# Kernel tuning notes

Hardware: AMD Instinct MI355X
Metric: run time of the kernel (lower is better)

Reference implementation:

```python
import jax, jax.numpy as jnp
import numpy as np

# Stand-in base model config (HF-style causal LM)
L, D, H, DFF, V, T = 2, 1024, 16, 4096, 32000, 2
HD = D // H
B, S = 2, 1024


def setup_inputs() -> dict:
    key = jax.random.key(0)
    ks = jax.random.split(key, 20)
    s = 0.02
    ds = 0.002  # task-vector deltas are small finetuning differences
    inp = {
        "input_ids": jax.random.randint(ks[0], (B, S), 0, V, dtype=jnp.int32),
        "labels": jax.random.randint(ks[1], (B, S), 0, V, dtype=jnp.int32),
        "lambdas": jax.random.uniform(ks[2], (T,), jnp.float32) * 0.5,
        # base parameters (frozen, like base_model)
        "emb": jax.random.normal(ks[3], (V, D), jnp.float32) * s,
        "Wqkv": jax.random.normal(ks[4], (L, D, 3 * D), jnp.float32) * s,
        "Wo": jax.random.normal(ks[5], (L, D, D), jnp.float32) * s,
        "W1": jax.random.normal(ks[6], (L, D, DFF), jnp.float32) * s,
        "W2": jax.random.normal(ks[7], (L, DFF, D), jnp.float32) * s,
        "g1": jnp.ones((L, D), jnp.float32),
        "g2": jnp.ones((L, D), jnp.float32),
        "gf": jnp.ones((D,), jnp.float32),
        # stacked task-vector deltas: leading dim T (one slice per CPUStoredTaskVector)
        "d_emb": jax.random.normal(ks[8], (T, V, D), jnp.float32) * ds,
        "d_Wqkv": jax.random.normal(ks[9], (T, L, D, 3 * D), jnp.float32) * ds,
        "d_Wo": jax.random.normal(ks[10], (T, L, D, D), jnp.float32) * ds,
        "d_W1": jax.random.normal(ks[11], (T, L, D, DFF), jnp.float32) * ds,
        "d_W2": jax.random.normal(ks[12], (T, L, DFF, D), jnp.float32) * ds,
        "d_g1": jax.random.normal(ks[13], (T, L, D), jnp.float32) * ds,
        "d_g2": jax.random.normal(ks[14], (T, L, D), jnp.float32) * ds,
        "d_gf": jax.random.normal(ks[15], (T, D), jnp.float32) * ds,
    }
    return inp


def _ln(x, g):
    mu = x.mean(-1, keepdims=True)
    var = ((x - mu) ** 2).mean(-1, keepdims=True)
    return (x - mu) * jax.lax.rsqrt(var + 1e-5) * g


def reference(input_ids, labels, lambdas, emb, Wqkv, Wo, W1, W2, g1, g2, gf,
              d_emb, d_Wqkv, d_Wo, d_W1, d_W2, d_g1, d_g2, d_gf):
    # fused layerwise merge: param + sum_i lambdas[i] * delta_i (single pass over all deltas)
    m = lambda base, d: base + jnp.einsum("t,t...->...", lambdas, d)
    emb_m = m(emb, d_emb)
    x = emb_m[input_ids]  # [B, S, D]
    b, s, _ = x.shape
    causal = jnp.tril(jnp.ones((s, s), bool))

    def body(h, p):
        wqkv, wo, w1, w2, gg1, gg2 = p
        a = _ln(h, gg1)
        qkv = a @ wqkv  # [B,S,3D]
        q, k, v = jnp.split(qkv, 3, axis=-1)
        q = q.reshape(b, s, H, HD)
        k = k.reshape(b, s, H, HD)
        v = v.reshape(b, s, H, HD)
        att = jnp.einsum("bqhd,bkhd->bhqk", q, k) / jnp.sqrt(jnp.float32(HD))
        att = jnp.where(causal, att, jnp.float32(-1e9))
        att = jax.nn.softmax(att, axis=-1)
        o = jnp.einsum("bhqk,bkhd->bqhd", att, v).reshape(b, s, D)
        h = h + o @ wo
        a = _ln(h, gg2)
        h = h + jax.nn.gelu(a @ w1) @ w2
        return h, None

    merged = (m(Wqkv, d_Wqkv), m(Wo, d_Wo), m(W1, d_W1), m(W2, d_W2),
              m(g1, d_g1), m(g2, d_g2))
    x, _ = jax.lax.scan(body, x, merged)
    x = _ln(x, m(gf, d_gf))
    logits = x @ emb_m.T  # tied embeddings, [B,S,V]
    # HF causal-LM loss: shift logits left, labels right
    logp = jax.nn.log_softmax(logits[:, :-1, :], axis=-1)
    tgt = labels[:, 1:]
    nll = -jnp.take_along_axis(logp, tgt[..., None].astype(jnp.int32), axis=-1)[..., 0]
    return nll.mean()
```

## Files before the change

### kernel.cpp

```cpp
#include <hip/hip_runtime.h>
#include <math.h>

#define L_ 2
#define D_ 1024
#define H_ 16
#define HD_ 64
#define DFF_ 4096
#define V_ 32000
#define B_ 2
#define S_ 1024
#define BS_ (B_*S_)
#define D3_ (3*D_)
#define VC_ 6400

typedef __attribute__((ext_vector_type(8))) short short8;
typedef __attribute__((ext_vector_type(4))) float f32x4;
typedef __attribute__((ext_vector_type(4))) unsigned int uint4v;

__device__ __forceinline__ float b2f(unsigned short u) {
    return __uint_as_float(((unsigned int)u) << 16);
}
__device__ __forceinline__ unsigned short f2b(float f) {
    unsigned int u = __float_as_uint(f);
    return (unsigned short)((u + 0x7fffu + ((u >> 16) & 1u)) >> 16);
}
__device__ __forceinline__ float blo(unsigned int u) { return __uint_as_float(u << 16); }
__device__ __forceinline__ float bhi(unsigned int u) { return __uint_as_float(u & 0xffff0000u); }

__device__ __forceinline__ void gld16(const void* g, void* l) {
    __builtin_amdgcn_global_load_lds(
        (const __attribute__((address_space(1))) unsigned int*)g,
        (__attribute__((address_space(3))) unsigned int*)l, 16, 0, 0);
}


__global__ void merge_f32_kernel(const float* __restrict__ base, const float* __restrict__ dlt,
                                 size_t tstride, const float* __restrict__ lam,
                                 float* __restrict__ out, int n) {
    float l0 = lam[0], l1 = lam[1];
    for (int i = blockIdx.x * blockDim.x + threadIdx.x; i < n; i += gridDim.x * blockDim.x)
        out[i] = base[i] + l0 * dlt[i] + l1 * dlt[i + tstride];
}

__global__ void merge_bf16_kernel(const float* __restrict__ base, const float* __restrict__ dlt,
                                  size_t tstride, const float* __restrict__ lam,
                                  unsigned short* __restrict__ out, size_t n4) {
    float l0 = lam[0], l1 = lam[1];
    for (size_t q = blockIdx.x * blockDim.x + threadIdx.x; q < n4; q += (size_t)gridDim.x * blockDim.x) {
        size_t i = q * 4;
        float4 b = *(const float4*)(base + i);
        float4 d0 = *(const float4*)(dlt + i);
        float4 d1 = *(const float4*)(dlt + tstride + i);
        ushort4 o;
        o.x = f2b(b.x + l0 * d0.x + l1 * d1.x);
        o.y = f2b(b.y + l0 * d0.y + l1 * d1.y);
        o.z = f2b(b.z + l0 * d0.z + l1 * d1.z);
        o.w = f2b(b.w + l0 * d0.w + l1 * d1.w);
        *(ushort4*)(out + i) = o;
    }
}

__global__ __launch_bounds__(256) void mt_kernel(const float* __restrict__ in,
                                                 const float* __restrict__ din, size_t tstride,
                                                 const float* __restrict__ lam,
                                                 unsigned short* __restrict__ outT,
                                                 int K, int N) {
    __shared__ float T[64][65];
    float l0 = lam[0], l1 = lam[1];
    int n0 = blockIdx.x * 64, k0 = blockIdx.y * 64;
    int tr = threadIdx.x >> 4;
    int tc = threadIdx.x & 15;
    #pragma unroll
    for (int rep = 0; rep < 4; rep++) {
        int kk = tr + rep * 16;
        size_t idx = (size_t)(k0 + kk) * N + n0 + tc * 4;
        float4 b = *(const float4*)(in + idx);
        float4 d0 = *(const float4*)(din + idx);
        float4 d1 = *(const float4*)(din + tstride + idx);
        T[kk][tc * 4 + 0] = b.x + l0 * d0.x + l1 * d1.x;
        T[kk][tc * 4 + 1] = b.y + l0 * d0.y + l1 * d1.y;
        T[kk][tc * 4 + 2] = b.z + l0 * d0.z + l1 * d1.z;
        T[kk][tc * 4 + 3] = b.w + l0 * d0.w + l1 * d1.w;
    }
    __syncthreads();
    #pragma unroll
    for (int rep = 0; rep < 4; rep++) {
        int n = tr + rep * 16;
        int kc = tc * 4;
        ushort4 o;
        o.x = f2b(T[kc + 0][n]);
        o.y = f2b(T[kc + 1][n]);
        o.z = f2b(T[kc + 2][n]);
        o.w = f2b(T[kc + 3][n]);
        *(ushort4*)(outT + (size_t)(n0 + n) * K + k0 + kc) = o;
    }
}


__global__ void embed_kernel(const int* __restrict__ ids, const unsigned short* __restrict__ embm,
                             float* __restrict__ h) {
    int row = blockIdx.x;
    int id = ids[row];
    const unsigned short* src = embm + (size_t)id * D_;
    float* dst = h + (size_t)row * D_;
    for (int d = threadIdx.x; d < D_; d += 256) dst[d] = b2f(src[d]);
}

__global__ __launch_bounds__(256) void ln_kernel(const float* __restrict__ x,
                                                 const float* __restrict__ g,
                                                 unsigned short* __restrict__ out) {
    __shared__ float sred[8];
    int row = blockIdx.x;
    const float* xr = x + (size_t)row * D_;
    float s = 0.f, ss = 0.f;
    for (int d = threadIdx.x; d < D_; d += 256) { float v = xr[d]; s += v; ss += v * v; }
    for (int o = 32; o > 0; o >>= 1) { s += __shfl_down(s, o); ss += __shfl_down(ss, o); }
    int lane = threadIdx.x & 63, wid = threadIdx.x >> 6;
    if (lane == 0) { sred[wid] = s; sred[4 + wid] = ss; }
    __syncthreads();
    if (threadIdx.x == 0) {
        sred[0] = sred[0] + sred[1] + sred[2] + sred[3];
        sred[4] = sred[4] + sred[5] + sred[6] + sred[7];
    }
    __syncthreads();
    float mu = sred[0] * (1.0f / D_);
    float var = sred[4] * (1.0f / D_) - mu * mu;
    float r = rsqrtf(var + 1e-5f);
    unsigned short* orow = out + (size_t)row * D_;
    for (int d = threadIdx.x; d < D_; d += 256) orow[d] = f2b((xr[d] - mu) * r * g[d]);
}

template<int MODE>
__global__ __launch_bounds__(256) void gemm_mfma(const unsigned short* __restrict__ A,
                                                 const unsigned short* __restrict__ Bt,
                                                 float* __restrict__ Cf,
                                                 unsigned short* __restrict__ Cb,
                                                 int M, int N, int K) {
    __shared__ unsigned short As[128 * 32];
    __shared__ unsigned short Bs[128 * 32];
    int bm = blockIdx.y * 128, bn = blockIdx.x * 128;
    int tid = threadIdx.x;
    int w = tid >> 6, lane = tid & 63;
    int wm = (w & 1) * 64, wn = (w >> 1) * 64;
    int l15 = lane & 15, quad = lane >> 4;
    f32x4 acc[4][4] = {};

    int arow = w * 32 + (lane >> 2);
    int aseg = (lane & 3) * 8;
    const unsigned short* gA0 = A + (size_t)(bm + arow) * K + aseg;
    const unsigned short* gA1 = A + (size_t)(bm + arow + 16) * K + aseg;
    const unsigned short* gB0 = Bt + (size_t)(bn + arow) * K + aseg;
    const unsigned short* gB1 = Bt + (size_t)(bn + arow + 16) * K + aseg;
    unsigned short* lA0 = &As[arow * 32 + aseg];
    unsigned short* lA1 = &As[(arow + 16) * 32 + aseg];
    unsigned short* lB0 = &Bs[arow * 32 + aseg];
    unsigned short* lB1 = &Bs[(arow + 16) * 32 + aseg];

    for (int k0 = 0; k0 < K; k0 += 32) {
        gld16(gA0 + k0, lA0);
        gld16(gA1 + k0, lA1);
        gld16(gB0 + k0, lB0);
        gld16(gB1 + k0, lB1);
        __syncthreads();
        short8 af[4], bfm[4];
        #pragma unroll
        for (int i = 0; i < 4; i++) af[i] = *(const short8*)&As[(wm + i * 16 + l15) * 32 + quad * 8];
        #pragma unroll
        for (int j = 0; j < 4; j++) bfm[j] = *(const short8*)&Bs[(wn + j * 16 + l15) * 32 + quad * 8];
        #pragma unroll
        for (int i = 0; i < 4; i++)
            #pragma unroll
            for (int j = 0; j < 4; j++)
                acc[i][j] = __builtin_amdgcn_mfma_f32_16x16x32_bf16(af[i], bfm[j], acc[i][j], 0, 0, 0);
        __syncthreads();
    }

    #pragma unroll
    for (int i = 0; i < 4; i++) {
        int row = bm + wm + i * 16 + quad * 4;
        #pragma unroll
        for (int j = 0; j < 4; j++) {
            int col = bn + wn + j * 16 + l15;
            #pragma unroll
            for (int r = 0; r < 4; r++) {
                size_t idx = (size_t)(row + r) * N + col;
                float v = acc[i][j][r];
                if (MODE == 0) Cf[idx] = v;
                if (MODE == 1) Cf[idx] += v;
                if (MODE == 2) Cb[idx] = f2b(v);
                if (MODE == 3) {
                    float c = 0.7978845608028654f * (v + 0.044715f * v * v * v);
                    Cb[idx] = f2b(0.5f * v * (1.0f + tanhf(c)));
                }
            }
        }
    }
}

#define UNPACK8(u, dst) { (dst)[0]=blo((u).x);(dst)[1]=bhi((u).x);(dst)[2]=blo((u).y);(dst)[3]=bhi((u).y);(dst)[4]=blo((u).z);(dst)[5]=bhi((u).z);(dst)[6]=blo((u).w);(dst)[7]=bhi((u).w); }

__global__ __launch_bounds__(256) void attn_kernel(const unsigned short* __restrict__ qkv,
                                                   unsigned short* __restrict__ attno) {
    int qt = blockIdx.x, h = blockIdx.y, b = blockIdx.z;
    int tid = threadIdx.x;
    int w = tid >> 6, lane = tid & 63;
    int l15 = lane & 15, quad = lane >> 4;

    __shared__ unsigned short Ks[64][72];
    __shared__ float Vt[64][68];
    __shared__ unsigned short Ps[4][16][72];

    short8 aq[2];
    {
        const unsigned short* gq = qkv + (size_t)(b * S_ + qt * 64 + w * 16 + l15) * D3_ + h * HD_ + quad * 8;
        aq[0] = *(const short8*)(gq);
        aq[1] = *(const short8*)(gq + 32);
    }

    f32x4 oacc[4] = {};
    float m_i[4] = {-1e30f, -1e30f, -1e30f, -1e30f};
    float l_i[4] = {0.f, 0.f, 0.f, 0.f};

    int krr = tid >> 3, kseg = tid & 7;
    int vrr = tid >> 2, vd0 = (tid & 3) * 16;

    for (int kt = 0; kt <= qt; kt++) {
        __syncthreads();
        {
            const unsigned short* gk = qkv + (size_t)(b * S_ + kt * 64 + krr) * D3_ + D_ + h * HD_ + kseg * 8;
            uint4 u0 = *(const uint4*)gk;
            uint4 u1 = *(const uint4*)(gk + (size_t)32 * D3_);
            *(uint4*)&Ks[krr][kseg * 8] = u0;
            *(uint4*)&Ks[krr + 32][kseg * 8] = u1;
        }
        {
            const unsigned short* gv = qkv + (size_t)(b * S_ + kt * 64 + vrr) * D3_ + 2 * D_ + h * HD_ + vd0;
            uint4 v0 = *(const uint4*)gv;
            uint4 v1 = *(const uint4*)(gv + 8);
            float tmp[16];
            UNPACK8(v0, tmp); UNPACK8(v1, tmp + 8);
            #pragma unroll
            for (int u = 0; u < 16; u++) Vt[vd0 + u][vrr] = tmp[u];
        }
        __syncthreads();

        f32x4 sc[4] = {};
        #pragma unroll
        for (int kk = 0; kk < 2; kk++)
            #pragma unroll
            for (int j = 0; j < 4; j++) {
                short8 bk = *(const short8*)&Ks[j * 16 + l15][kk * 32 + quad * 8];
                sc[j] = __builtin_amdgcn_mfma_f32_16x16x32_bf16(aq[kk], bk, sc[j], 0, 0, 0);
            }

        bool diag = (kt == qt);
        #pragma unroll
        for (int j = 0; j < 4; j++)
            #pragma unroll
            for (int r = 0; r < 4; r++) {
                float v = sc[j][r] * 0.125f;
                if (diag && (j * 16 + l15) > (w * 16 + quad * 4 + r)) v = -1e30f;
                sc[j][r] = v;
            }

        #pragma unroll
        for (int r = 0; r < 4; r++) {
            float rm = fmaxf(fmaxf(sc[0][r], sc[1][r]), fmaxf(sc[2][r], sc[3][r]));
            rm = fmaxf(rm, __shfl_xor(rm, 1));
            rm = fmaxf(rm, __shfl_xor(rm, 2));
            rm = fmaxf(rm, __shfl_xor(rm, 4));
            rm = fmaxf(rm, __shfl_xor(rm, 8));
            float mnew = fmaxf(m_i[r], rm);
            float alpha = __expf(m_i[r] - mnew);
            float p0 = __expf(sc[0][r] - mnew);
            float p1 = __expf(sc[1][r] - mnew);
            float p2 = __expf(sc[2][r] - mnew);
            float p3 = __expf(sc[3][r] - mnew);
            float ls = p0 + p1 + p2 + p3;
            ls += __shfl_xor(ls, 1);
            ls += __shfl_xor(ls, 2);
            ls += __shfl_xor(ls, 4);
            ls += __shfl_xor(ls, 8);
            l_i[r] = l_i[r] * alpha + ls;
            m_i[r] = mnew;
            oacc[0][r] *= alpha; oacc[1][r] *= alpha;
            oacc[2][r] *= alpha; oacc[3][r] *= alpha;
            Ps[w][quad * 4 + r][ 0 + l15] = f2b(p0);
            Ps[w][quad * 4 + r][16 + l15] = f2b(p1);
            Ps[w][quad * 4 + r][32 + l15] = f2b(p2);
            Ps[w][quad * 4 + r][48 + l15] = f2b(p3);
        }

        #pragma unroll
        for (int kk = 0; kk < 2; kk++) {
            short8 pa = *(const short8*)&Ps[w][l15][kk * 32 + quad * 8];
            #pragma unroll
            for (int j = 0; j < 4; j++) {
                const float* vp = &Vt[j * 16 + l15][kk * 32 + quad * 8];
                f32x4 f0 = *(const f32x4*)vp;
                f32x4 f1 = *(const f32x4*)(vp + 4);
                unsigned int b0 = (__float_as_uint(f0[1]) & 0xffff0000u) | (__float_as_uint(f0[0]) >> 16);
                unsigned int b1 = (__float_as_uint(f0[3]) & 0xffff0000u) | (__float_as_uint(f0[2]) >> 16);
                unsigned int b2 = (__float_as_uint(f1[1]) & 0xffff0000u) | (__float_as_uint(f1[0]) >> 16);
                unsigned int b3 = (__float_as_uint(f1[3]) & 0xffff0000u) | (__float_as_uint(f1[2]) >> 16);
                union { uint4v u; short8 s; } cvt;
                cvt.u = (uint4v){b0, b1, b2, b3};
                oacc[j] = __builtin_amdgcn_mfma_f32_16x16x32_bf16(pa, cvt.s, oacc[j], 0, 0, 0);
            }
        }
    }

    #pragma unroll
    for (int r = 0; r < 4; r++) {
        float inv = 1.0f / l_i[r];
        size_t row = (size_t)(b * S_ + qt * 64 + w * 16 + quad * 4 + r);
        #pragma unroll
        for (int j = 0; j < 4; j++)
            attno[row * D_ + h * HD_ + j * 16 + l15] = f2b(oacc[j][r] * inv);
    }
}


__global__ void loss_init_kernel(float* rm, float* rl, float* rtl) {
    int i = blockIdx.x * blockDim.x + threadIdx.x;
    if (i < BS_) { rm[i] = -1e30f; rl[i] = 0.f; rtl[i] = 0.f; }
}

__global__ __launch_bounds__(256) void loss_chunk_kernel(const float* __restrict__ lg,
                                                         const int* __restrict__ labels,
                                                         float* rm, float* rl, float* rtl,
                                                         int v0) {
    int row = blockIdx.x;
    const float* lr = lg + (size_t)row * VC_;
    int tid = threadIdx.x;
    __shared__ float sred[8];
    float m = -1e30f;
    for (int j = tid; j < VC_; j += 256) m = fmaxf(m, lr[j]);
    for (int o = 32; o > 0; o >>= 1) m = fmaxf(m, __shfl_down(m, o));
    int lane = tid & 63, wid = tid >> 6;
    if (lane == 0) sred[wid] = m;
    __syncthreads();
    if (tid == 0) sred[0] = fmaxf(fmaxf(sred[0], sred[1]), fmaxf(sred[2], sred[3]));
    __syncthreads();
    float cm = sred[0];
    float s = 0.f;
    for (int j = tid; j < VC_; j += 256) s += __expf(lr[j] - cm);
    for (int o = 32; o > 0; o >>= 1) s += __shfl_down(s, o);
    if (lane == 0) sred[4 + wid] = s;
    __syncthreads();
    if (tid == 0) {
        float cs = sred[4] + sred[5] + sred[6] + sred[7];
        float om = rm[row], ol = rl[row];
        float nm = fmaxf(om, cm);
        rl[row] = ol * __expf(om - nm) + cs * __expf(cm - nm);
        rm[row] = nm;
        int b = row / S_, spos = row % S_;
        if (spos < S_ - 1) {
            int tgt = labels[b * S_ + spos + 1];
            if (tgt >= v0 && tgt < v0 + VC_) rtl[row] = lr[tgt - v0];
        }
    }
}

__global__ __launch_bounds__(256) void loss_final_kernel(const float* rm, const float* rl,
                                                         const float* rtl, float* out) {
    __shared__ float sred[4];
    float s = 0.f;
    for (int row = threadIdx.x; row < BS_; row += 256) {
        int spos = row % S_;
        if (spos < S_ - 1) s += (rm[row] + logf(rl[row])) - rtl[row];
    }
    for (int o = 32; o > 0; o >>= 1) s += __shfl_down(s, o);
    int lane = threadIdx.x & 63, wid = threadIdx.x >> 6;
    if (lane == 0) sred[wid] = s;
    __syncthreads();
    if (threadIdx.x == 0)
        out[0] = (sred[0] + sred[1] + sred[2] + sred[3]) * (1.0f / (B_ * (S_ - 1)));
}


extern "C" void kernel_launch(void* const* d_in, const int* in_sizes, int n_in,
                              void* d_out, int out_size, void* d_ws, size_t ws_size,
                              hipStream_t stream) {
    const int*   ids    = (const int*)d_in[0];
    const int*   labels = (const int*)d_in[1];
    const float* lam    = (const float*)d_in[2];
    const float* emb    = (const float*)d_in[3];
    const float* Wqkv   = (const float*)d_in[4];
    const float* Wo     = (const float*)d_in[5];
    const float* W1     = (const float*)d_in[6];
    const float* W2     = (const float*)d_in[7];
    const float* g1     = (const float*)d_in[8];
    const float* g2     = (const float*)d_in[9];
    const float* gf     = (const float*)d_in[10];
    const float* dEmb   = (const float*)d_in[11];
    const float* dWqkv  = (const float*)d_in[12];
    const float* dWo    = (const float*)d_in[13];
    const float* dW1    = (const float*)d_in[14];
    const float* dW2    = (const float*)d_in[15];
    const float* dG1    = (const float*)d_in[16];
    const float* dG2    = (const float*)d_in[17];
    const float* dGf    = (const float*)d_in[18];
    float* out = (float*)d_out;

    char* wsb = (char*)d_ws;
    size_t off = 0;
    auto alloc = [&](size_t bytes) {
        off = (off + 255) & ~(size_t)255;
        void* p = wsb + off;
        off += bytes;
        return p;
    };
    unsigned short* embm  = (unsigned short*)alloc((size_t)V_ * D_ * 2);
    unsigned short* WqkvT = (unsigned short*)alloc((size_t)L_ * D3_ * D_ * 2);
    unsigned short* WoT   = (unsigned short*)alloc((size_t)L_ * D_ * D_ * 2);
    unsigned short* W1T   = (unsigned short*)alloc((size_t)L_ * DFF_ * D_ * 2);
    unsigned short* W2T   = (unsigned short*)alloc((size_t)L_ * D_ * DFF_ * 2);
    float* g1m = (float*)alloc((size_t)L_ * D_ * 4);
    float* g2m = (float*)alloc((size_t)L_ * D_ * 4);
    float* gfm = (float*)alloc((size_t)D_ * 4);
    float* h   = (float*)alloc((size_t)BS_ * D_ * 4);
    unsigned short* a_bf  = (unsigned short*)alloc((size_t)BS_ * D_ * 2);
    unsigned short* qkv   = (unsigned short*)alloc((size_t)BS_ * D3_ * 2);
    unsigned short* attno = (unsigned short*)alloc((size_t)BS_ * D_ * 2);
    unsigned short* ffh   = (unsigned short*)alloc((size_t)BS_ * DFF_ * 2);
    float* lchunk = (float*)alloc((size_t)BS_ * VC_ * 4);
    float* rm  = (float*)alloc(BS_ * 4);
    float* rl  = (float*)alloc(BS_ * 4);
    float* rtl = (float*)alloc(BS_ * 4);

    merge_bf16_kernel<<<4096, 256, 0, stream>>>(emb, dEmb, (size_t)V_ * D_, lam, embm, (size_t)V_ * D_ / 4);
    for (int l = 0; l < L_; l++) {
        mt_kernel<<<dim3(D3_ / 64, D_ / 64), 256, 0, stream>>>(
            Wqkv + (size_t)l * D_ * D3_, dWqkv + (size_t)l * D_ * D3_, (size_t)L_ * D_ * D3_,
            lam, WqkvT + (size_t)l * D3_ * D_, D_, D3_);
        mt_kernel<<<dim3(D_ / 64, D_ / 64), 256, 0, stream>>>(
            Wo + (size_t)l * D_ * D_, dWo + (size_t)l * D_ * D_, (size_t)L_ * D_ * D_,
            lam, WoT + (size_t)l * D_ * D_, D_, D_);
        mt_kernel<<<dim3(DFF_ / 64, D_ / 64), 256, 0, stream>>>(
            W1 + (size_t)l * D_ * DFF_, dW1 + (size_t)l * D_ * DFF_, (size_t)L_ * D_ * DFF_,
            lam, W1T + (size_t)l * DFF_ * D_, D_, DFF_);
        mt_kernel<<<dim3(D_ / 64, DFF_ / 64), 256, 0, stream>>>(
            W2 + (size_t)l * DFF_ * D_, dW2 + (size_t)l * DFF_ * D_, (size_t)L_ * DFF_ * D_,
            lam, W2T + (size_t)l * D_ * DFF_, DFF_, D_);
    }
    merge_f32_kernel<<<8, 256, 0, stream>>>(g1, dG1, (size_t)L_ * D_, lam, g1m, L_ * D_);
    merge_f32_kernel<<<8, 256, 0, stream>>>(g2, dG2, (size_t)L_ * D_, lam, g2m, L_ * D_);
    merge_f32_kernel<<<4, 256, 0, stream>>>(gf, dGf, (size_t)D_, lam, gfm, D_);

    embed_kernel<<<BS_, 256, 0, stream>>>(ids, embm, h);

    for (int l = 0; l < L_; l++) {
        ln_kernel<<<BS_, 256, 0, stream>>>(h, g1m + l * D_, a_bf);
        gemm_mfma<2><<<dim3(D3_ / 128, BS_ / 128), 256, 0, stream>>>(
            a_bf, WqkvT + (size_t)l * D3_ * D_, nullptr, qkv, BS_, D3_, D_);
        attn_kernel<<<dim3(S_ / 64, H_, B_), 256, 0, stream>>>(qkv, attno);
        gemm_mfma<1><<<dim3(D_ / 128, BS_ / 128), 256, 0, stream>>>(
            attno, WoT + (size_t)l * D_ * D_, h, nullptr, BS_, D_, D_);
        ln_kernel<<<BS_, 256, 0, stream>>>(h, g2m + l * D_, a_bf);
        gemm_mfma<3><<<dim3(DFF_ / 128, BS_ / 128), 256, 0, stream>>>(
            a_bf, W1T + (size_t)l * DFF_ * D_, nullptr, ffh, BS_, DFF_, D_);
        gemm_mfma<1><<<dim3(D_ / 128, BS_ / 128), 256, 0, stream>>>(
            ffh, W2T + (size_t)l * D_ * DFF_, h, nullptr, BS_, D_, DFF_);
    }

    ln_kernel<<<BS_, 256, 0, stream>>>(h, gfm, a_bf);

    loss_init_kernel<<<(BS_ + 255) / 256, 256, 0, stream>>>(rm, rl, rtl);
    for (int c = 0; c < V_ / VC_; c++) {
        int v0 = c * VC_;
        gemm_mfma<0><<<dim3(VC_ / 128, BS_ / 128), 256, 0, stream>>>(
            a_bf, embm + (size_t)v0 * D_, lchunk, nullptr, BS_, VC_, D_);
        loss_chunk_kernel<<<BS_, 256, 0, stream>>>(lchunk, labels, rm, rl, rtl, v0);
    }
    loss_final_kernel<<<1, 256, 0, stream>>>(rm, rl, rtl, out);
}
```

Baseline: 1.615 ms.

## Fuse LM-head GEMM with online log-softmax partials, drop logits buffer

Replaces the chunked logits GEMM plus per-chunk loss passes with one GEMM kernel that computes per-128-column max and sum-exp partials and captures the target logit in its epilogue. A row kernel merges the 250 partials per row, and a final kernel sums the per-row NLL. This removes writing and re-reading the large fp32 logits buffer and many kernel launches. It adds an extra exp and shuffle reduction in the GEMM epilogue.

```diff
diff --git a/kernel.cpp b/kernel.cpp
--- a/kernel.cpp
+++ b/kernel.cpp
@@ -11,7 +11,7 @@
 #define S_ 1024
 #define BS_ (B_*S_)
 #define D3_ (3*D_)
-#define VC_ 6400
+#define NT_ (V_/128)
 
 typedef __attribute__((ext_vector_type(8))) short short8;
 typedef __attribute__((ext_vector_type(4))) float f32x4;
@@ -185,7 +185,6 @@
             for (int r = 0; r < 4; r++) {
                 size_t idx = (size_t)(row + r) * N + col;
                 float v = acc[i][j][r];
-                if (MODE == 0) Cf[idx] = v;
                 if (MODE == 1) Cf[idx] += v;
                 if (MODE == 2) Cb[idx] = f2b(v);
                 if (MODE == 3) {
@@ -195,6 +194,140 @@
             }
         }
     }
+}
+
+__global__ __launch_bounds__(256) void gemm_loss_kernel(const unsigned short* __restrict__ A,
+                                                        const unsigned short* __restrict__ Bt,
+                                                        const int* __restrict__ labels,
+                                                        float2* __restrict__ part,
+                                                        float* __restrict__ rtl) {
+    __shared__ unsigned short As[128 * 32];
+    __shared__ unsigned short Bs[128 * 32];
+    __shared__ float Ms[128][2];
+    __shared__ float Ls[128][2];
+    __shared__ int tgts[128];
+    const int K = D_;
+    int bm = blockIdx.y * 128, bn = blockIdx.x * 128;
+    int tid = threadIdx.x;
+    int w = tid >> 6, lane = tid & 63;
+    int wm = (w & 1) * 64, wn = (w >> 1) * 64;
+    int l15 = lane & 15, quad = lane >> 4;
+    f32x4 acc[4][4] = {};
+
+    int arow = w * 32 + (lane >> 2);
+    int aseg = (lane & 3) * 8;
+    const unsigned short* gA0 = A + (size_t)(bm + arow) * K + aseg;
+    const unsigned short* gA1 = A + (size_t)(bm + arow + 16) * K + aseg;
+    const unsigned short* gB0 = Bt + (size_t)(bn + arow) * K + aseg;
+    const unsigned short* gB1 = Bt + (size_t)(bn + arow + 16) * K + aseg;
+    unsigned short* lA0 = &As[arow * 32 + aseg];
+    unsigned short* lA1 = &As[(arow + 16) * 32 + aseg];
+    unsigned short* lB0 = &Bs[arow * 32 + aseg];
+    unsigned short* lB1 = &Bs[(arow + 16) * 32 + aseg];
+
+    for (int k0 = 0; k0 < K; k0 += 32) {
+        gld16(gA0 + k0, lA0);
+        gld16(gA1 + k0, lA1);
+        gld16(gB0 + k0, lB0);
+        gld16(gB1 + k0, lB1);
+        __syncthreads();
+        short8 af[4], bfm[4];
+        #pragma unroll
+        for (int i = 0; i < 4; i++) af[i] = *(const short8*)&As[(wm + i * 16 + l15) * 32 + quad * 8];
+        #pragma unroll
+        for (int j = 0; j < 4; j++) bfm[j] = *(const short8*)&Bs[(wn + j * 16 + l15) * 32 + quad * 8];
+        #pragma unroll
+        for (int i = 0; i < 4; i++)
+            #pragma unroll
+            for (int j = 0; j < 4; j++)
+                acc[i][j] = __builtin_amdgcn_mfma_f32_16x16x32_bf16(af[i], bfm[j], acc[i][j], 0, 0, 0);
+        __syncthreads();
+    }
+
+    if (tid < 128) {
+        int rg = bm + tid;
+        int b = rg / S_, spos = rg % S_;
+        tgts[tid] = (spos < S_ - 1) ? labels[b * S_ + spos + 1] : -1;
+    }
+    __syncthreads();
+
+    #pragma unroll
+    for (int i = 0; i < 4; i++) {
+        #pragma unroll
+        for (int r = 0; r < 4; r++) {
+            int rowl = wm + i * 16 + quad * 4 + r;
+            int tgt = tgts[rowl];
+            float m = fmaxf(fmaxf(acc[i][0][r], acc[i][1][r]), fmaxf(acc[i][2][r], acc[i][3][r]));
+            m = fmaxf(m, __shfl_xor(m, 1));
+            m = fmaxf(m, __shfl_xor(m, 2));
+            m = fmaxf(m, __shfl_xor(m, 4));
+            m = fmaxf(m, __shfl_xor(m, 8));
+            float l = 0.f;
+            #pragma unroll
+            for (int j = 0; j < 4; j++) {
+                float v = acc[i][j][r];
+                l += __expf(v - m);
+                if (bn + wn + j * 16 + l15 == tgt) rtl[bm + rowl] = v;
+            }
+            l += __shfl_xor(l, 1);
+            l += __shfl_xor(l, 2);
+            l += __shfl_xor(l, 4);
+            l += __shfl_xor(l, 8);
+            if (l15 == 0) { Ms[rowl][w >> 1] = m; Ls[rowl][w >> 1] = l; }
+        }
+    }
+    __syncthreads();
+    if (tid < 128) {
+        float m0 = Ms[tid][0], m1 = Ms[tid][1];
+        float l0 = Ls[tid][0], l1 = Ls[tid][1];
+        float m = fmaxf(m0, m1);
+        float l = l0 * __expf(m0 - m) + l1 * __expf(m1 - m);
+        part[(size_t)(bm + tid) * NT_ + blockIdx.x] = make_float2(m, l);
+    }
+}
+
+__global__ __launch_bounds__(256) void loss_row_kernel(const float2* __restrict__ part,
+                                                       const float* __restrict__ rtl,
+                                                       float* __restrict__ rnll) {
+    int row = blockIdx.x;
+    int tid = threadIdx.x;
+    float m = -1e30f, l = 0.f;
+    if (tid < NT_) { float2 p = part[(size_t)row * NT_ + tid]; m = p.x; l = p.y; }
+    #pragma unroll
+    for (int o = 1; o < 64; o <<= 1) {
+        float mo = __shfl_xor(m, o), lo = __shfl_xor(l, o);
+        float nm = fmaxf(m, mo);
+        l = l * __expf(m - nm) + lo * __expf(mo - nm);
+        m = nm;
+    }
+    __shared__ float sm[4], sl[4];
+    int lane = tid & 63, wid = tid >> 6;
+    if (lane == 0) { sm[wid] = m; sl[wid] = l; }
+    __syncthreads();
+    if (tid == 0) {
+        float M = sm[0], L = sl[0];
+        #pragma unroll
+        for (int i = 1; i < 4; i++) {
+            float nm = fmaxf(M, sm[i]);
+            L = L * __expf(M - nm) + sl[i] * __expf(sm[i] - nm);
+            M = nm;
+        }
+        int spos = row % S_;
+        rnll[row] = (spos < S_ - 1) ? (M + logf(L)) - rtl[row] : 0.f;
+    }
+}
+
+__global__ __launch_bounds__(256) void loss_sum_kernel(const float* __restrict__ rnll,
+                                                       float* __restrict__ out) {
+    __shared__ float sred[4];
+    float s = 0.f;
+    for (int row = threadIdx.x; row < BS_; row += 256) s += rnll[row];
+    for (int o = 32; o > 0; o >>= 1) s += __shfl_down(s, o);
+    int lane = threadIdx.x & 63, wid = threadIdx.x >> 6;
+    if (lane == 0) sred[wid] = s;
+    __syncthreads();
+    if (threadIdx.x == 0)
+        out[0] = (sred[0] + sred[1] + sred[2] + sred[3]) * (1.0f / (B_ * (S_ - 1)));
 }
 
 #define UNPACK8(u, dst) { (dst)[0]=blo((u).x);(dst)[1]=bhi((u).x);(dst)[2]=blo((u).y);(dst)[3]=bhi((u).y);(dst)[4]=blo((u).z);(dst)[5]=bhi((u).z);(dst)[6]=blo((u).w);(dst)[7]=bhi((u).w); }
@@ -321,64 +454,6 @@
 }
 
 
-__global__ void loss_init_kernel(float* rm, float* rl, float* rtl) {
-    int i = blockIdx.x * blockDim.x + threadIdx.x;
-    if (i < BS_) { rm[i] = -1e30f; rl[i] = 0.f; rtl[i] = 0.f; }
-}
-
-__global__ __launch_bounds__(256) void loss_chunk_kernel(const float* __restrict__ lg,
-                                                         const int* __restrict__ labels,
-                                                         float* rm, float* rl, float* rtl,
-                                                         int v0) {
-    int row = blockIdx.x;
-    const float* lr = lg + (size_t)row * VC_;
-    int tid = threadIdx.x;
-    __shared__ float sred[8];
-    float m = -1e30f;
-    for (int j = tid; j < VC_; j += 256) m = fmaxf(m, lr[j]);
-    for (int o = 32; o > 0; o >>= 1) m = fmaxf(m, __shfl_down(m, o));
-    int lane = tid & 63, wid = tid >> 6;
-    if (lane == 0) sred[wid] = m;
-    __syncthreads();
-    if (tid == 0) sred[0] = fmaxf(fmaxf(sred[0], sred[1]), fmaxf(sred[2], sred[3]));
-    __syncthreads();
-    float cm = sred[0];
-    float s = 0.f;
-    for (int j = tid; j < VC_; j += 256) s += __expf(lr[j] - cm);
-    for (int o = 32; o > 0; o >>= 1) s += __shfl_down(s, o);
-    if (lane == 0) sred[4 + wid] = s;
-    __syncthreads();
-    if (tid == 0) {
-        float cs = sred[4] + sred[5] + sred[6] + sred[7];
-        float om = rm[row], ol = rl[row];
-        float nm = fmaxf(om, cm);
-        rl[row] = ol * __expf(om - nm) + cs * __expf(cm - nm);
-        rm[row] = nm;
-        int b = row / S_, spos = row % S_;
-        if (spos < S_ - 1) {
-            int tgt = labels[b * S_ + spos + 1];
-            if (tgt >= v0 && tgt < v0 + VC_) rtl[row] = lr[tgt - v0];
-        }
-    }
-}
-
-__global__ __launch_bounds__(256) void loss_final_kernel(const float* rm, const float* rl,
-                                                         const float* rtl, float* out) {
-    __shared__ float sred[4];
-    float s = 0.f;
-    for (int row = threadIdx.x; row < BS_; row += 256) {
-        int spos = row % S_;
-        if (spos < S_ - 1) s += (rm[row] + logf(rl[row])) - rtl[row];
-    }
-    for (int o = 32; o > 0; o >>= 1) s += __shfl_down(s, o);
-    int lane = threadIdx.x & 63, wid = threadIdx.x >> 6;
-    if (lane == 0) sred[wid] = s;
-    __syncthreads();
-    if (threadIdx.x == 0)
-        out[0] = (sred[0] + sred[1] + sred[2] + sred[3]) * (1.0f / (B_ * (S_ - 1)));
-}
-
-
 extern "C" void kernel_launch(void* const* d_in, const int* in_sizes, int n_in,
                               void* d_out, int out_size, void* d_ws, size_t ws_size,
                               hipStream_t stream) {
@@ -424,10 +499,9 @@
     unsigned short* qkv   = (unsigned short*)alloc((size_t)BS_ * D3_ * 2);
     unsigned short* attno = (unsigned short*)alloc((size_t)BS_ * D_ * 2);
     unsigned short* ffh   = (unsigned short*)alloc((size_t)BS_ * DFF_ * 2);
-    float* lchunk = (float*)alloc((size_t)BS_ * VC_ * 4);
-    float* rm  = (float*)alloc(BS_ * 4);
-    float* rl  = (float*)alloc(BS_ * 4);
-    float* rtl = (float*)alloc(BS_ * 4);
+    float2* part = (float2*)alloc((size_t)BS_ * NT_ * 8);
+    float* rtl  = (float*)alloc(BS_ * 4);
+    float* rnll = (float*)alloc(BS_ * 4);
 
     merge_bf16_kernel<<<4096, 256, 0, stream>>>(emb, dEmb, (size_t)V_ * D_, lam, embm, (size_t)V_ * D_ / 4);
     for (int l = 0; l < L_; l++) {
@@ -466,12 +540,7 @@
 
     ln_kernel<<<BS_, 256, 0, stream>>>(h, gfm, a_bf);
 
-    loss_init_kernel<<<(BS_ + 255) / 256, 256, 0, stream>>>(rm, rl, rtl);
-    for (int c = 0; c < V_ / VC_; c++) {
-        int v0 = c * VC_;
-        gemm_mfma<0><<<dim3(VC_ / 128, BS_ / 128), 256, 0, stream>>>(
-            a_bf, embm + (size_t)v0 * D_, lchunk, nullptr, BS_, VC_, D_);
-        loss_chunk_kernel<<<BS_, 256, 0, stream>>>(lchunk, labels, rm, rl, rtl, v0);
-    }
-    loss_final_kernel<<<1, 256, 0, stream>>>(rm, rl, rtl, out);
-}
+    gemm_loss_kernel<<<dim3(NT_, BS_ / 128), 256, 0, stream>>>(a_bf, embm, labels, part, rtl);
+    loss_row_kernel<<<BS_, 256, 0, stream>>>(part, rtl, rnll);
+    loss_sum_kernel<<<1, 256, 0, stream>>>(rnll, out);
+}
```

New measurement: 1.444 ms. 10.6% less time.
